# Optimization experiments

Measured on AMD Instinct MI355X. Metric: run time of the kernel, lower is better.

The kernel has to match this reference:

```python
import jax, jax.numpy as jnp
import numpy as np

# CSSA config (index=0): H=W=64, strip windows h_spa=64, w_spa=8, heads=4, C=64
B, HW, C, HEADS = 32, 64, 64, 4
HS, WS = 64, 8          # h_spa, w_spa
HD = C // HEADS          # head_dim = 16
WIN = HS * WS            # 512 tokens per window
SCALE = HD ** -0.5


def setup_inputs() -> dict:
    key = jax.random.key(0)
    k1, k2, k3 = jax.random.split(key, 3)
    qkv = jax.random.normal(k1, (3, B, HW * HW, C), dtype=jnp.float32)
    w_conv = jax.random.normal(k2, (C, 1, 3, 3), dtype=jnp.float32) * 0.1
    b_conv = jax.random.normal(k3, (C,), dtype=jnp.float32) * 0.1
    return {"qkv": qkv, "w_conv": w_conv, "b_conv": b_conv}


def _to_img(x):
    # [B, N, C] -> [B, C, H, W]
    return jnp.transpose(x.reshape(B, HW, HW, C), (0, 3, 1, 2))


def _img2window_heads(x):
    img = _to_img(x)
    img = img.reshape(B, C, HW // HS, HS, HW // WS, WS)
    win = jnp.transpose(img, (0, 2, 4, 3, 5, 1)).reshape(-1, WIN, C)
    return jnp.transpose(win.reshape(-1, WIN, HEADS, HD), (0, 2, 1, 3))


def _v_windows(x):
    # [B, N, C] -> [B*nWin, C, h_spa, w_spa] (image-layout windows for conv)
    img = _to_img(x)
    img = img.reshape(B, C, HW // HS, HS, HW // WS, WS)
    return jnp.transpose(img, (0, 2, 4, 1, 3, 5)).reshape(-1, C, HS, WS)


def reference(qkv, w_conv, b_conv):
    q, k, v = qkv[0], qkv[1], qkv[2]
    qh = _img2window_heads(q) * SCALE
    kh = _img2window_heads(k)
    vw = _v_windows(v)                           # [Bw, C, HS, WS]
    # depthwise 3x3 conv LePE
    lepe = jax.lax.conv_general_dilated(
        vw, w_conv, window_strides=(1, 1), padding=((1, 1), (1, 1)),
        feature_group_count=C,
        dimension_numbers=("NCHW", "OIHW", "NCHW")) + b_conv[None, :, None, None]
    Bw = vw.shape[0]
    lepe = jnp.transpose(lepe.reshape(Bw, HEADS, HD, WIN), (0, 1, 3, 2))
    vh = jnp.transpose(vw.reshape(Bw, HEADS, HD, WIN), (0, 1, 3, 2))
    attn = jax.nn.softmax(jnp.einsum("whqd,whkd->whqk", qh, kh), axis=-1)
    x = jnp.einsum("whqk,whkd->whqd", attn, vh) + lepe
    x = jnp.transpose(x, (0, 2, 1, 3)).reshape(Bw, WIN, C)
    # window2spa
    x = x.reshape(B, HW // HS, HW // WS, HS, WS, C)
    x = jnp.transpose(x, (0, 1, 3, 2, 4, 5)).reshape(B, HW * HW, C)
    return x
```

## Files before the change

kernel.cpp:

```cpp
#include <hip/hip_runtime.h>
#include <stdint.h>

#define KSTR2 20
#define VSTR  520

typedef __attribute__((ext_vector_type(4))) short          short4v;
typedef __attribute__((ext_vector_type(4))) float          f32x4;
typedef __attribute__((ext_vector_type(4))) unsigned short us4;
typedef __bf16 bf2_t __attribute__((ext_vector_type(2)));

__device__ __forceinline__ unsigned short f2bf(float f) {
    union { float f; unsigned int u; } x; x.f = f;
    return (unsigned short)((x.u + 0x8000u) >> 16);
}
__device__ __forceinline__ float bf2f(unsigned short u) {
    union { unsigned int i; float f; } x; x.i = ((unsigned int)u) << 16; return x.f;
}
__device__ __forceinline__ unsigned int pk2bf(float lo, float hi) {
#if __has_builtin(__builtin_amdgcn_cvt_pk_bf16_f32)
    union { bf2_t v; unsigned int u; } c;
    c.v = __builtin_amdgcn_cvt_pk_bf16_f32(lo, hi);
    return c.u;
#else
    union { float f; unsigned int u; } a, b; a.f = lo; b.f = hi;
    return __builtin_amdgcn_perm(b.u + 0x8000u, a.u + 0x8000u, 0x07060302u);
#endif
}
__device__ __forceinline__ short4v pk4bf(float a, float b, float c, float d) {
    union { short4v s; unsigned int u[2]; } p;
    p.u[0] = pk2bf(a, b);
    p.u[1] = pk2bf(c, d);
    return p.s;
}

__global__ __launch_bounds__(512, 6)
void CSSA_69355131896243_kernel(const float* __restrict__ qkv,
                                const float* __restrict__ wconv,
                                const float* __restrict__ bconv,
                                float* __restrict__ out)
{
    __shared__ unsigned short Kl[512 * KSTR2];
    __shared__ unsigned short Vt[16 * VSTR];
    __shared__ float Wl[144];
    __shared__ float Bl[16];

    const int tid  = threadIdx.x;
    const int wave = tid >> 6, lane = tid & 63, quad = lane >> 4, l15 = lane & 15;

    const int bid = blockIdx.x;
    const int win = (bid & 7) * 32 + (bid >> 5);
    const int h   = (bid >> 3) & 3;
    const int b   = win >> 3, wx = win & 7;

    const size_t ONE  = (size_t)32 * 4096 * 64;
    const size_t base = ((size_t)b * 4096 + (size_t)wx * 8) * 64;
    const float* gQ = qkv + base;
    const float* gK = qkv + ONE + base;
    const float* gV = qkv + 2 * ONE + base;
    const int hc = h * 16;

    {
        const int c4 = tid & 3;
        const int t0 = tid >> 2;
        #pragma unroll
        for (int r = 0; r < 4; ++r) {
            const int t = r * 128 + t0;
            const size_t goff = (size_t)(t >> 3) * 4096 + (size_t)(t & 7) * 64 + hc + c4 * 4;
            f32x4 kd = *(const f32x4*)(gK + goff);
            f32x4 vd = *(const f32x4*)(gV + goff);
            us4 kb;
            #pragma unroll
            for (int j = 0; j < 4; ++j) kb[j] = f2bf(kd[j]);
            *(us4*)(&Kl[t * KSTR2 + c4 * 4]) = kb;
            #pragma unroll
            for (int j = 0; j < 4; ++j) Vt[(c4 * 4 + j) * VSTR + t] = f2bf(vd[j]);
        }
    }
    if (tid < 144) Wl[tid] = wconv[h * 144 + tid];
    if (tid < 16)  Bl[tid] = bconv[hc + tid];

    const float SCL = 0.25f * 1.44269504088896341f;
    const int q0 = wave * 64;
    short4v qf[4];
    #pragma unroll
    for (int t = 0; t < 4; ++t) {
        const int q = q0 + t * 16 + l15;
        f32x4 qv = *(const f32x4*)(gQ + (size_t)(q >> 3) * 4096 + (size_t)(q & 7) * 64 + hc + quad * 4);
        qf[t] = pk4bf(qv[0] * SCL, qv[1] * SCL, qv[2] * SCL, qv[3] * SCL);
    }
    __syncthreads();

    f32x4 acc[4];
    float lp[4];
    #pragma unroll
    for (int t = 0; t < 4; ++t) { acc[t] = (f32x4)0.0f; lp[t] = 0.0f; }

    #pragma unroll 4
    for (int c = 0; c < 32; ++c) {
        const short4v kf = *(const short4v*)(&Kl[(c * 16 + l15) * KSTR2 + quad * 4]);
        const short4v vf = *(const short4v*)(&Vt[l15 * VSTR + c * 16 + quad * 4]);
        #pragma unroll
        for (int t = 0; t < 4; ++t) {
            f32x4 s = __builtin_amdgcn_mfma_f32_16x16x16bf16_1k(kf, qf[t], (f32x4)0.0f, 0, 0, 0);
            const float p0 = __builtin_amdgcn_exp2f(s[0]);
            const float p1 = __builtin_amdgcn_exp2f(s[1]);
            const float p2 = __builtin_amdgcn_exp2f(s[2]);
            const float p3 = __builtin_amdgcn_exp2f(s[3]);
            lp[t] += (p0 + p1) + (p2 + p3);
            acc[t] = __builtin_amdgcn_mfma_f32_16x16x16bf16_1k(vf, pk4bf(p0, p1, p2, p3), acc[t], 0, 0, 0);
        }
    }

    float linv[4];
    #pragma unroll
    for (int t = 0; t < 4; ++t) {
        float v = lp[t];
        v += __shfl_xor(v, 16, 64);
        v += __shfl_xor(v, 32, 64);
        linv[t] = __builtin_amdgcn_rcpf(v);
    }

    #pragma unroll
    for (int j = 0; j < 4; ++j) {
        const int d = quad * 4 + j;
        float w9[9];
        #pragma unroll
        for (int o = 0; o < 9; ++o) w9[o] = Wl[d * 9 + o];
        const float bs = Bl[d];
        #pragma unroll
        for (int t = 0; t < 4; ++t) {
            const int q = q0 + t * 16 + l15;
            const int y = q >> 3, x = q & 7;
            float lep = bs;
            #pragma unroll
            for (int dy = 0; dy < 3; ++dy) {
                #pragma unroll
                for (int dx = 0; dx < 3; ++dx) {
                    const int yy = y + dy - 1, xx = x + dx - 1;
                    const bool ok = ((unsigned)yy < 64u) && ((unsigned)xx < 8u);
                    const int tt = (q + (dy - 1) * 8 + (dx - 1)) & 511;
                    lep += (ok ? w9[dy * 3 + dx] : 0.0f) * bf2f(Vt[d * VSTR + tt]);
                }
            }
            acc[t][j] = acc[t][j] * linv[t] + lep;
        }
    }
    float* gO = out + base;
    #pragma unroll
    for (int t = 0; t < 4; ++t) {
        const int q = q0 + t * 16 + l15;
        *(f32x4*)(gO + (size_t)(q >> 3) * 4096 + (size_t)(q & 7) * 64 + hc + quad * 4) = acc[t];
    }
}

extern "C" void kernel_launch(void* const* d_in, const int* in_sizes, int n_in,
                              void* d_out, int out_size, void* d_ws, size_t ws_size,
                              hipStream_t stream) {
    const float* qkv   = (const float*)d_in[0];
    const float* wconv = (const float*)d_in[1];
    const float* bconv = (const float*)d_in[2];
    float* outp = (float*)d_out;
    hipLaunchKernelGGL(CSSA_69355131896243_kernel, dim3(1024), dim3(512), 0, stream,
                       qkv, wconv, bconv, outp);
}
```

Before: 201.6 us.

## Use 16x16x32 bf16 MFMA for PV and re-layout K tiles in LDS

The P·V product now uses the 16x16x32 bf16 MFMA, so each iteration covers 32 keys with two QK MFMAs feeding one PV MFMA. This halves the PV instruction count and the number of loop iterations. K is stored in LDS in a swizzled, fragment-ordered layout with no padding, and V is read as 8-wide vectors. Conversions now use packed bf16 conversion, and the LePE conv indexes a zeroed padding slot instead of masking the weights. The K layout has to match the key ordering the PV MFMA expects, which is a correctness risk if the index mapping is wrong.

```diff
diff --git a/kernel.cpp b/kernel.cpp
--- a/kernel.cpp
+++ b/kernel.cpp
@@ -1,18 +1,15 @@
 #include <hip/hip_runtime.h>
 #include <stdint.h>
 
-#define KSTR2 20
-#define VSTR  520
+
+#define VSTR 520
 
 typedef __attribute__((ext_vector_type(4))) short          short4v;
 typedef __attribute__((ext_vector_type(4))) float          f32x4;
 typedef __attribute__((ext_vector_type(4))) unsigned short us4;
-typedef __bf16 bf2_t __attribute__((ext_vector_type(2)));
+typedef __bf16 bf2_t  __attribute__((ext_vector_type(2)));
+typedef __bf16 bf16x8 __attribute__((ext_vector_type(8)));
 
-__device__ __forceinline__ unsigned short f2bf(float f) {
-    union { float f; unsigned int u; } x; x.f = f;
-    return (unsigned short)((x.u + 0x8000u) >> 16);
-}
 __device__ __forceinline__ float bf2f(unsigned short u) {
     union { unsigned int i; float f; } x; x.i = ((unsigned int)u) << 16; return x.f;
 }
@@ -39,9 +36,9 @@
                                 const float* __restrict__ bconv,
                                 float* __restrict__ out)
 {
-    __shared__ unsigned short Kl[512 * KSTR2];
+    __shared__ unsigned short Kl[32 * 256];
     __shared__ unsigned short Vt[16 * VSTR];
-    __shared__ float Wl[144];
+    __shared__ float Wl[160];
     __shared__ float Bl[16];
 
     const int tid  = threadIdx.x;
@@ -68,15 +65,22 @@
             const size_t goff = (size_t)(t >> 3) * 4096 + (size_t)(t & 7) * 64 + hc + c4 * 4;
             f32x4 kd = *(const f32x4*)(gK + goff);
             f32x4 vd = *(const f32x4*)(gV + goff);
-            us4 kb;
-            #pragma unroll
-            for (int j = 0; j < 4; ++j) kb[j] = f2bf(kd[j]);
-            *(us4*)(&Kl[t * KSTR2 + c4 * 4]) = kb;
-            #pragma unroll
-            for (int j = 0; j < 4; ++j) Vt[(c4 * 4 + j) * VSTR + t] = f2bf(vd[j]);
+            union { us4 v; unsigned int u[2]; } kb;
+            kb.u[0] = pk2bf(kd[0], kd[1]);
+            kb.u[1] = pk2bf(kd[2], kd[3]);
+            const int cc = 2 * (t >> 5) + ((t >> 2) & 1);
+            const int m  = ((t >> 3) & 3) * 4 + (t & 3);
+            *(us4*)(&Kl[(cc * 4 + c4) * 64 + m * 4]) = kb.v;
+            const unsigned int v01 = pk2bf(vd[0], vd[1]);
+            const unsigned int v23 = pk2bf(vd[2], vd[3]);
+            Vt[(c4 * 4 + 0) * VSTR + t] = (unsigned short)(v01 & 0xffffu);
+            Vt[(c4 * 4 + 1) * VSTR + t] = (unsigned short)(v01 >> 16);
+            Vt[(c4 * 4 + 2) * VSTR + t] = (unsigned short)(v23 & 0xffffu);
+            Vt[(c4 * 4 + 3) * VSTR + t] = (unsigned short)(v23 >> 16);
         }
     }
-    if (tid < 144) Wl[tid] = wconv[h * 144 + tid];
+    if (tid < 16)  Vt[tid * VSTR + 512] = 0;
+    if (tid < 144) Wl[(tid / 9) * 10 + (tid % 9)] = wconv[h * 144 + tid];
     if (tid < 16)  Bl[tid] = bconv[hc + tid];
 
     const float SCL = 0.25f * 1.44269504088896341f;
@@ -95,19 +99,31 @@
     #pragma unroll
     for (int t = 0; t < 4; ++t) { acc[t] = (f32x4)0.0f; lp[t] = 0.0f; }
 
-    #pragma unroll 4
-    for (int c = 0; c < 32; ++c) {
-        const short4v kf = *(const short4v*)(&Kl[(c * 16 + l15) * KSTR2 + quad * 4]);
-        const short4v vf = *(const short4v*)(&Vt[l15 * VSTR + c * 16 + quad * 4]);
+    const unsigned short* Kf = &Kl[quad * 64 + l15 * 4];
+    const unsigned short* Vf = &Vt[l15 * VSTR + quad * 8];
+
+    #pragma unroll 2
+    for (int blk = 0; blk < 16; ++blk) {
+        const short4v kfA = *(const short4v*)(Kf + blk * 512);
+        const short4v kfB = *(const short4v*)(Kf + blk * 512 + 256);
+        const bf16x8 vf = *(const bf16x8*)(Vf + blk * 32);
         #pragma unroll
         for (int t = 0; t < 4; ++t) {
-            f32x4 s = __builtin_amdgcn_mfma_f32_16x16x16bf16_1k(kf, qf[t], (f32x4)0.0f, 0, 0, 0);
-            const float p0 = __builtin_amdgcn_exp2f(s[0]);
-            const float p1 = __builtin_amdgcn_exp2f(s[1]);
-            const float p2 = __builtin_amdgcn_exp2f(s[2]);
-            const float p3 = __builtin_amdgcn_exp2f(s[3]);
-            lp[t] += (p0 + p1) + (p2 + p3);
-            acc[t] = __builtin_amdgcn_mfma_f32_16x16x16bf16_1k(vf, pk4bf(p0, p1, p2, p3), acc[t], 0, 0, 0);
+            f32x4 sA = __builtin_amdgcn_mfma_f32_16x16x16bf16_1k(kfA, qf[t], (f32x4)0.0f, 0, 0, 0);
+            f32x4 sB = __builtin_amdgcn_mfma_f32_16x16x16bf16_1k(kfB, qf[t], (f32x4)0.0f, 0, 0, 0);
+            const float p0 = __builtin_amdgcn_exp2f(sA[0]);
+            const float p1 = __builtin_amdgcn_exp2f(sA[1]);
+            const float p2 = __builtin_amdgcn_exp2f(sA[2]);
+            const float p3 = __builtin_amdgcn_exp2f(sA[3]);
+            const float p4 = __builtin_amdgcn_exp2f(sB[0]);
+            const float p5 = __builtin_amdgcn_exp2f(sB[1]);
+            const float p6 = __builtin_amdgcn_exp2f(sB[2]);
+            const float p7 = __builtin_amdgcn_exp2f(sB[3]);
+            lp[t] += ((p0 + p1) + (p2 + p3)) + ((p4 + p5) + (p6 + p7));
+            union { bf16x8 v; unsigned int u[4]; } pb;
+            pb.u[0] = pk2bf(p0, p1); pb.u[1] = pk2bf(p2, p3);
+            pb.u[2] = pk2bf(p4, p5); pb.u[3] = pk2bf(p6, p7);
+            acc[t] = __builtin_amdgcn_mfma_f32_16x16x32_bf16(vf, pb.v, acc[t], 0, 0, 0);
         }
     }
 
@@ -120,26 +136,31 @@
         linv[t] = __builtin_amdgcn_rcpf(v);
     }
 
+    const int xb = l15 & 7;
     #pragma unroll
     for (int j = 0; j < 4; ++j) {
         const int d = quad * 4 + j;
         float w9[9];
         #pragma unroll
-        for (int o = 0; o < 9; ++o) w9[o] = Wl[d * 9 + o];
+        for (int o = 0; o < 9; ++o) w9[o] = Wl[d * 10 + o];
         const float bs = Bl[d];
+        const unsigned short* vrow = &Vt[d * VSTR];
         #pragma unroll
         for (int t = 0; t < 4; ++t) {
             const int q = q0 + t * 16 + l15;
-            const int y = q >> 3, x = q & 7;
+            const int y = q >> 3;
             float lep = bs;
             #pragma unroll
             for (int dy = 0; dy < 3; ++dy) {
+                const int yy  = y + dy - 1;
+                const bool oky = ((unsigned)yy < 64u);
+                const int yy8 = yy * 8;
                 #pragma unroll
                 for (int dx = 0; dx < 3; ++dx) {
-                    const int yy = y + dy - 1, xx = x + dx - 1;
-                    const bool ok = ((unsigned)yy < 64u) && ((unsigned)xx < 8u);
-                    const int tt = (q + (dy - 1) * 8 + (dx - 1)) & 511;
-                    lep += (ok ? w9[dy * 3 + dx] : 0.0f) * bf2f(Vt[d * VSTR + tt]);
+                    const int xx = xb + dx - 1;
+                    const bool ok = oky && ((unsigned)xx < 8u);
+                    const int ta = ok ? (yy8 + xx) : 512;
+                    lep += w9[dy * 3 + dx] * bf2f(vrow[ta]);
                 }
             }
             acc[t][j] = acc[t][j] * linv[t] + lep;
```

New measurement: 213.5 us. +5.9%, slower.

## Process all four heads per block with 1024-thread blocks over full windows

Applied to the files above, without the earlier changes.

Each block now handles one whole window across all four heads: 16 waves, each owning one head and 128 queries. K and V are staged once per window for all 64 channels, so each 16-channel global read is a full 256-byte row instead of a 64-byte slice per head block. The bf16 conversion now uses packed cvt. The trade-offs are larger LDS per block (about 135 KB), 8 accumulator tiles per wave (more register pressure), and only 256 blocks, which may under-fill the GPU and reduce latency hiding.

```diff
diff --git a/kernel.cpp b/kernel.cpp
--- a/kernel.cpp
+++ b/kernel.cpp
@@ -1,18 +1,14 @@
 #include <hip/hip_runtime.h>
 #include <stdint.h>
 
-#define KSTR2 20
-#define VSTR  520
+#define KSTR 68
+#define VSTR 520
 
 typedef __attribute__((ext_vector_type(4))) short          short4v;
 typedef __attribute__((ext_vector_type(4))) float          f32x4;
 typedef __attribute__((ext_vector_type(4))) unsigned short us4;
 typedef __bf16 bf2_t __attribute__((ext_vector_type(2)));
 
-__device__ __forceinline__ unsigned short f2bf(float f) {
-    union { float f; unsigned int u; } x; x.f = f;
-    return (unsigned short)((x.u + 0x8000u) >> 16);
-}
 __device__ __forceinline__ float bf2f(unsigned short u) {
     union { unsigned int i; float f; } x; x.i = ((unsigned int)u) << 16; return x.f;
 }
@@ -33,74 +29,76 @@
     return p.s;
 }
 
-__global__ __launch_bounds__(512, 6)
+__global__ __launch_bounds__(1024, 4)
 void CSSA_69355131896243_kernel(const float* __restrict__ qkv,
                                 const float* __restrict__ wconv,
                                 const float* __restrict__ bconv,
                                 float* __restrict__ out)
 {
-    __shared__ unsigned short Kl[512 * KSTR2];
-    __shared__ unsigned short Vt[16 * VSTR];
-    __shared__ float Wl[144];
-    __shared__ float Bl[16];
+    __shared__ unsigned short Kl[512 * KSTR];
+    __shared__ unsigned short Vt[64 * VSTR];
+    __shared__ float Wl[576];
+    __shared__ float Bl[64];
 
     const int tid  = threadIdx.x;
     const int wave = tid >> 6, lane = tid & 63, quad = lane >> 4, l15 = lane & 15;
 
     const int bid = blockIdx.x;
-    const int win = (bid & 7) * 32 + (bid >> 5);
-    const int h   = (bid >> 3) & 3;
-    const int b   = win >> 3, wx = win & 7;
+    const int b = bid >> 3, wx = bid & 7;
 
     const size_t ONE  = (size_t)32 * 4096 * 64;
     const size_t base = ((size_t)b * 4096 + (size_t)wx * 8) * 64;
     const float* gQ = qkv + base;
     const float* gK = qkv + ONE + base;
     const float* gV = qkv + 2 * ONE + base;
-    const int hc = h * 16;
 
     {
-        const int c4 = tid & 3;
-        const int t0 = tid >> 2;
+        const int c16 = tid & 15;
+        const int t0  = tid >> 4;
         #pragma unroll
-        for (int r = 0; r < 4; ++r) {
-            const int t = r * 128 + t0;
-            const size_t goff = (size_t)(t >> 3) * 4096 + (size_t)(t & 7) * 64 + hc + c4 * 4;
+        for (int r = 0; r < 8; ++r) {
+            const int t = r * 64 + t0;
+            const size_t goff = (size_t)(t >> 3) * 4096 + (size_t)(t & 7) * 64 + c16 * 4;
             f32x4 kd = *(const f32x4*)(gK + goff);
             f32x4 vd = *(const f32x4*)(gV + goff);
-            us4 kb;
-            #pragma unroll
-            for (int j = 0; j < 4; ++j) kb[j] = f2bf(kd[j]);
-            *(us4*)(&Kl[t * KSTR2 + c4 * 4]) = kb;
-            #pragma unroll
-            for (int j = 0; j < 4; ++j) Vt[(c4 * 4 + j) * VSTR + t] = f2bf(vd[j]);
+            union { us4 v; unsigned int u[2]; } kb;
+            kb.u[0] = pk2bf(kd[0], kd[1]);
+            kb.u[1] = pk2bf(kd[2], kd[3]);
+            *(us4*)(&Kl[t * KSTR + c16 * 4]) = kb.v;
+            const unsigned int v01 = pk2bf(vd[0], vd[1]);
+            const unsigned int v23 = pk2bf(vd[2], vd[3]);
+            Vt[(c16 * 4 + 0) * VSTR + t] = (unsigned short)(v01 & 0xffffu);
+            Vt[(c16 * 4 + 1) * VSTR + t] = (unsigned short)(v01 >> 16);
+            Vt[(c16 * 4 + 2) * VSTR + t] = (unsigned short)(v23 & 0xffffu);
+            Vt[(c16 * 4 + 3) * VSTR + t] = (unsigned short)(v23 >> 16);
         }
     }
-    if (tid < 144) Wl[tid] = wconv[h * 144 + tid];
-    if (tid < 16)  Bl[tid] = bconv[hc + tid];
+    if (tid < 576) Wl[tid] = wconv[tid];
+    if (tid < 64)  Bl[tid] = bconv[tid];
 
     const float SCL = 0.25f * 1.44269504088896341f;
-    const int q0 = wave * 64;
-    short4v qf[4];
+    const int h  = wave & 3, hc = h * 16;
+    const int q0 = (wave >> 2) * 128;
+    short4v qf[8];
     #pragma unroll
-    for (int t = 0; t < 4; ++t) {
+    for (int t = 0; t < 8; ++t) {
         const int q = q0 + t * 16 + l15;
         f32x4 qv = *(const f32x4*)(gQ + (size_t)(q >> 3) * 4096 + (size_t)(q & 7) * 64 + hc + quad * 4);
         qf[t] = pk4bf(qv[0] * SCL, qv[1] * SCL, qv[2] * SCL, qv[3] * SCL);
     }
     __syncthreads();
 
-    f32x4 acc[4];
-    float lp[4];
+    f32x4 acc[8];
+    float lp[8];
     #pragma unroll
-    for (int t = 0; t < 4; ++t) { acc[t] = (f32x4)0.0f; lp[t] = 0.0f; }
+    for (int t = 0; t < 8; ++t) { acc[t] = (f32x4)0.0f; lp[t] = 0.0f; }
 
-    #pragma unroll 4
+    #pragma unroll 2
     for (int c = 0; c < 32; ++c) {
-        const short4v kf = *(const short4v*)(&Kl[(c * 16 + l15) * KSTR2 + quad * 4]);
-        const short4v vf = *(const short4v*)(&Vt[l15 * VSTR + c * 16 + quad * 4]);
+        const short4v kf = *(const short4v*)(&Kl[(c * 16 + l15) * KSTR + hc + quad * 4]);
+        const short4v vf = *(const short4v*)(&Vt[(hc + l15) * VSTR + c * 16 + quad * 4]);
         #pragma unroll
-        for (int t = 0; t < 4; ++t) {
+        for (int t = 0; t < 8; ++t) {
             f32x4 s = __builtin_amdgcn_mfma_f32_16x16x16bf16_1k(kf, qf[t], (f32x4)0.0f, 0, 0, 0);
             const float p0 = __builtin_amdgcn_exp2f(s[0]);
             const float p1 = __builtin_amdgcn_exp2f(s[1]);
@@ -111,9 +109,9 @@
         }
     }
 
-    float linv[4];
+    float linv[8];
     #pragma unroll
-    for (int t = 0; t < 4; ++t) {
+    for (int t = 0; t < 8; ++t) {
         float v = lp[t];
         v += __shfl_xor(v, 16, 64);
         v += __shfl_xor(v, 32, 64);
@@ -122,13 +120,14 @@
 
     #pragma unroll
     for (int j = 0; j < 4; ++j) {
-        const int d = quad * 4 + j;
+        const int d = hc + quad * 4 + j;
         float w9[9];
         #pragma unroll
         for (int o = 0; o < 9; ++o) w9[o] = Wl[d * 9 + o];
         const float bs = Bl[d];
+        const unsigned short* vrow = &Vt[d * VSTR];
         #pragma unroll
-        for (int t = 0; t < 4; ++t) {
+        for (int t = 0; t < 8; ++t) {
             const int q = q0 + t * 16 + l15;
             const int y = q >> 3, x = q & 7;
             float lep = bs;
@@ -139,7 +138,7 @@
                     const int yy = y + dy - 1, xx = x + dx - 1;
                     const bool ok = ((unsigned)yy < 64u) && ((unsigned)xx < 8u);
                     const int tt = (q + (dy - 1) * 8 + (dx - 1)) & 511;
-                    lep += (ok ? w9[dy * 3 + dx] : 0.0f) * bf2f(Vt[d * VSTR + tt]);
+                    lep += (ok ? w9[dy * 3 + dx] : 0.0f) * bf2f(vrow[tt]);
                 }
             }
             acc[t][j] = acc[t][j] * linv[t] + lep;
@@ -147,7 +146,7 @@
     }
     float* gO = out + base;
     #pragma unroll
-    for (int t = 0; t < 4; ++t) {
+    for (int t = 0; t < 8; ++t) {
         const int q = q0 + t * 16 + l15;
         *(f32x4*)(gO + (size_t)(q >> 3) * 4096 + (size_t)(q & 7) * 64 + hc + quad * 4) = acc[t];
     }
@@ -160,6 +159,6 @@
     const float* wconv = (const float*)d_in[1];
     const float* bconv = (const float*)d_in[2];
     float* outp = (float*)d_out;
-    hipLaunchKernelGGL(CSSA_69355131896243_kernel, dim3(1024), dim3(512), 0, stream,
+    hipLaunchKernelGGL(CSSA_69355131896243_kernel, dim3(256), dim3(1024), 0, stream,
                        qkv, wconv, bconv, outp);
 }
```

New measurement: 215.7 us. 1.07x slower.

## Process two heads per 1024-thread block with wider coalesced K/V loads

Applied to the files above, without the earlier changes.

Each block now handles a pair of heads (32 channels) for one window using 1024 threads, so the block grid halves. Global K/V loads cover 32 contiguous floats per token instead of 16, which improves coalescing, and each wave picks its head through an offset into shared memory. The float-to-bf16 conversion now uses a packed convert, and the LDS strides are changed. In exchange each block uses more LDS and more threads, which can reduce the number of resident blocks and change occupancy.

```diff
diff --git a/kernel.cpp b/kernel.cpp
--- a/kernel.cpp
+++ b/kernel.cpp
@@ -1,18 +1,14 @@
 #include <hip/hip_runtime.h>
 #include <stdint.h>
 
-#define KSTR2 20
-#define VSTR  520
+#define KSTR 36
+#define VSTR 516
 
 typedef __attribute__((ext_vector_type(4))) short          short4v;
 typedef __attribute__((ext_vector_type(4))) float          f32x4;
 typedef __attribute__((ext_vector_type(4))) unsigned short us4;
 typedef __bf16 bf2_t __attribute__((ext_vector_type(2)));
 
-__device__ __forceinline__ unsigned short f2bf(float f) {
-    union { float f; unsigned int u; } x; x.f = f;
-    return (unsigned short)((x.u + 0x8000u) >> 16);
-}
 __device__ __forceinline__ float bf2f(unsigned short u) {
     union { unsigned int i; float f; } x; x.i = ((unsigned int)u) << 16; return x.f;
 }
@@ -33,59 +29,65 @@
     return p.s;
 }
 
-__global__ __launch_bounds__(512, 6)
+__global__ __launch_bounds__(1024, 8)
 void CSSA_69355131896243_kernel(const float* __restrict__ qkv,
                                 const float* __restrict__ wconv,
                                 const float* __restrict__ bconv,
                                 float* __restrict__ out)
 {
-    __shared__ unsigned short Kl[512 * KSTR2];
-    __shared__ unsigned short Vt[16 * VSTR];
-    __shared__ float Wl[144];
-    __shared__ float Bl[16];
+    __shared__ unsigned short Kl[512 * KSTR];
+    __shared__ unsigned short Vt[32 * VSTR];
+    __shared__ float Wl[288];
+    __shared__ float Bl[32];
 
     const int tid  = threadIdx.x;
     const int wave = tid >> 6, lane = tid & 63, quad = lane >> 4, l15 = lane & 15;
 
     const int bid = blockIdx.x;
-    const int win = (bid & 7) * 32 + (bid >> 5);
-    const int h   = (bid >> 3) & 3;
+    const int p   = (bid >> 3) & 1;
+    const int win = (bid & 7) * 32 + (bid >> 4);
     const int b   = win >> 3, wx = win & 7;
+    const int pc  = p * 32;
 
     const size_t ONE  = (size_t)32 * 4096 * 64;
     const size_t base = ((size_t)b * 4096 + (size_t)wx * 8) * 64;
     const float* gQ = qkv + base;
     const float* gK = qkv + ONE + base;
     const float* gV = qkv + 2 * ONE + base;
-    const int hc = h * 16;
 
     {
-        const int c4 = tid & 3;
-        const int t0 = tid >> 2;
+        const int c8 = tid & 7;
+        const int t0 = tid >> 3;
         #pragma unroll
         for (int r = 0; r < 4; ++r) {
             const int t = r * 128 + t0;
-            const size_t goff = (size_t)(t >> 3) * 4096 + (size_t)(t & 7) * 64 + hc + c4 * 4;
+            const size_t goff = (size_t)(t >> 3) * 4096 + (size_t)(t & 7) * 64 + pc + c8 * 4;
             f32x4 kd = *(const f32x4*)(gK + goff);
             f32x4 vd = *(const f32x4*)(gV + goff);
-            us4 kb;
-            #pragma unroll
-            for (int j = 0; j < 4; ++j) kb[j] = f2bf(kd[j]);
-            *(us4*)(&Kl[t * KSTR2 + c4 * 4]) = kb;
-            #pragma unroll
-            for (int j = 0; j < 4; ++j) Vt[(c4 * 4 + j) * VSTR + t] = f2bf(vd[j]);
+            union { us4 v; unsigned int u[2]; } kb;
+            kb.u[0] = pk2bf(kd[0], kd[1]);
+            kb.u[1] = pk2bf(kd[2], kd[3]);
+            *(us4*)(&Kl[t * KSTR + c8 * 4]) = kb.v;
+            const unsigned int v01 = pk2bf(vd[0], vd[1]);
+            const unsigned int v23 = pk2bf(vd[2], vd[3]);
+            Vt[(c8 * 4 + 0) * VSTR + t] = (unsigned short)(v01 & 0xffffu);
+            Vt[(c8 * 4 + 1) * VSTR + t] = (unsigned short)(v01 >> 16);
+            Vt[(c8 * 4 + 2) * VSTR + t] = (unsigned short)(v23 & 0xffffu);
+            Vt[(c8 * 4 + 3) * VSTR + t] = (unsigned short)(v23 >> 16);
         }
     }
-    if (tid < 144) Wl[tid] = wconv[h * 144 + tid];
-    if (tid < 16)  Bl[tid] = bconv[hc + tid];
+    if (tid < 288) Wl[tid] = wconv[p * 288 + tid];
+    if (tid < 32)  Bl[tid] = bconv[pc + tid];
 
     const float SCL = 0.25f * 1.44269504088896341f;
-    const int q0 = wave * 64;
+    const int hl  = (wave & 1) * 16;
+    const int hg  = pc + hl;
+    const int q0  = (wave >> 1) * 64;
     short4v qf[4];
     #pragma unroll
     for (int t = 0; t < 4; ++t) {
         const int q = q0 + t * 16 + l15;
-        f32x4 qv = *(const f32x4*)(gQ + (size_t)(q >> 3) * 4096 + (size_t)(q & 7) * 64 + hc + quad * 4);
+        f32x4 qv = *(const f32x4*)(gQ + (size_t)(q >> 3) * 4096 + (size_t)(q & 7) * 64 + hg + quad * 4);
         qf[t] = pk4bf(qv[0] * SCL, qv[1] * SCL, qv[2] * SCL, qv[3] * SCL);
     }
     __syncthreads();
@@ -97,8 +99,8 @@
 
     #pragma unroll 4
     for (int c = 0; c < 32; ++c) {
-        const short4v kf = *(const short4v*)(&Kl[(c * 16 + l15) * KSTR2 + quad * 4]);
-        const short4v vf = *(const short4v*)(&Vt[l15 * VSTR + c * 16 + quad * 4]);
+        const short4v kf = *(const short4v*)(&Kl[(c * 16 + l15) * KSTR + hl + quad * 4]);
+        const short4v vf = *(const short4v*)(&Vt[(hl + l15) * VSTR + c * 16 + quad * 4]);
         #pragma unroll
         for (int t = 0; t < 4; ++t) {
             f32x4 s = __builtin_amdgcn_mfma_f32_16x16x16bf16_1k(kf, qf[t], (f32x4)0.0f, 0, 0, 0);
@@ -122,11 +124,12 @@
 
     #pragma unroll
     for (int j = 0; j < 4; ++j) {
-        const int d = quad * 4 + j;
+        const int dl = hl + quad * 4 + j;
         float w9[9];
         #pragma unroll
-        for (int o = 0; o < 9; ++o) w9[o] = Wl[d * 9 + o];
-        const float bs = Bl[d];
+        for (int o = 0; o < 9; ++o) w9[o] = Wl[dl * 9 + o];
+        const float bs = Bl[dl];
+        const unsigned short* vrow = &Vt[dl * VSTR];
         #pragma unroll
         for (int t = 0; t < 4; ++t) {
             const int q = q0 + t * 16 + l15;
@@ -139,7 +142,7 @@
                     const int yy = y + dy - 1, xx = x + dx - 1;
                     const bool ok = ((unsigned)yy < 64u) && ((unsigned)xx < 8u);
                     const int tt = (q + (dy - 1) * 8 + (dx - 1)) & 511;
-                    lep += (ok ? w9[dy * 3 + dx] : 0.0f) * bf2f(Vt[d * VSTR + tt]);
+                    lep += (ok ? w9[dy * 3 + dx] : 0.0f) * bf2f(vrow[tt]);
                 }
             }
             acc[t][j] = acc[t][j] * linv[t] + lep;
@@ -149,7 +152,7 @@
     #pragma unroll
     for (int t = 0; t < 4; ++t) {
         const int q = q0 + t * 16 + l15;
-        *(f32x4*)(gO + (size_t)(q >> 3) * 4096 + (size_t)(q & 7) * 64 + hc + quad * 4) = acc[t];
+        *(f32x4*)(gO + (size_t)(q >> 3) * 4096 + (size_t)(q & 7) * 64 + hg + quad * 4) = acc[t];
     }
 }
 
@@ -160,6 +163,6 @@
     const float* wconv = (const float*)d_in[1];
     const float* bconv = (const float*)d_in[2];
     float* outp = (float*)d_out;
-    hipLaunchKernelGGL(CSSA_69355131896243_kernel, dim3(1024), dim3(512), 0, stream,
+    hipLaunchKernelGGL(CSSA_69355131896243_kernel, dim3(512), dim3(1024), 0, stream,
                        qkv, wconv, bconv, outp);
 }
```

Measured after the change: 248.8 us. +23.4%, slower.
